# Performance work log

Measured on AMD Instinct MI355X. Metric: run time of the kernel, lower is better.

Reference implementation:

```python
import jax, jax.numpy as jnp
import numpy as np

NEG_INF = -1.0e9  # matches masked_fill_(mask, -1e9)


def setup_inputs() -> dict:
    key = jax.random.key(0)
    k1, k2, k3, k4 = jax.random.split(key, 4)
    B, Tq, Tk, D = 16, 2048, 2048, 1024
    q = jax.random.normal(k1, (B, Tq, D), dtype=jnp.float32)
    k = jax.random.normal(k2, (B, D, Tk), dtype=jnp.float32)  # pre-transposed keys (proj_k output layout)
    v = jax.random.normal(k3, (B, Tk, D), dtype=jnp.float32)
    mask = jax.random.randint(k4, (B, Tq, Tk), 0, 2).astype(jnp.bool_)
    return {"q": q, "k": k, "v": v, "mask": mask}


def reference(q, k, v, mask):
    # scores: [B, Tq, Tk]
    scores = jnp.einsum('bqd,bdk->bqk', q, k)
    scores = jnp.where(mask, jnp.asarray(NEG_INF, scores.dtype), scores)
    att = jax.nn.softmax(scores, axis=-1)
    # dropout is identity in eval mode (training=False)
    context = jnp.einsum('bqk,bkd->bqd', att, v)
    return context
```

## Files before the change

### kernel.cpp

```cpp
#include <hip/hip_runtime.h>
#include <hip/hip_fp16.h>


#define B_    16
#define TQ    2048
#define TK    2048
#define DH    1024
#define BQ    64
#define BT    256
#define DC    128
#define NTHR  512
#define NEG_INF_ -1.0e9f

typedef __attribute__((ext_vector_type(8))) _Float16  f16x8;
typedef __attribute__((ext_vector_type(4))) _Float16  f16x4;
typedef __attribute__((ext_vector_type(4))) float     f32x4;
typedef unsigned int   u32;
typedef unsigned short u16;

__global__ void detect_mask_kernel(const void* __restrict__ mask, int* flag_out) {
    const int tid = threadIdx.x;
    const int*   mi = (const int*)mask;
    const float* mf = (const float*)mask;
    int ok_i = 1, ok_f = 1;
    for (int k = 0; k < 16; ++k) {
        int idx = tid * 16 + k;
        int iv = mi[idx];
        ok_i &= ((iv == 0) | (iv == 1));
        float fv = mf[idx];
        ok_f &= ((fv == 0.0f) | (fv == 1.0f));
    }
    int all_i = __syncthreads_and(ok_i);
    int all_f = __syncthreads_and(ok_f);
    if (tid == 0) flag_out[0] = all_i ? 0 : (all_f ? 1 : 2);
}

template<int CTRL>
__device__ __forceinline__ float dpp_rot(float x) {
    return __int_as_float(__builtin_amdgcn_update_dpp(
        0, __float_as_int(x), CTRL, 0xf, 0xf, false));
}
__device__ __forceinline__ float rowmax16(float v) {
    v = fmaxf(v, dpp_rot<0x128>(v));
    v = fmaxf(v, dpp_rot<0x124>(v));
    v = fmaxf(v, dpp_rot<0x122>(v));
    v = fmaxf(v, dpp_rot<0x121>(v));
    return v;
}
__device__ __forceinline__ float rowsum16(float v) {
    v += dpp_rot<0x128>(v);
    v += dpp_rot<0x124>(v);
    v += dpp_rot<0x122>(v);
    v += dpp_rot<0x121>(v);
    return v;
}

__device__ __forceinline__ void gl_lds16(const u16* g, u16* l) {
    __builtin_amdgcn_global_load_lds(
        (const __attribute__((address_space(1))) u32*)(const void*)g,
        (__attribute__((address_space(3))) u32*)(void*)l, 16, 0, 0);
}

__global__ __launch_bounds__(256)
void prep_q(const float* __restrict__ Q, u16* __restrict__ Qh, u16* __restrict__ Ql) {
    const size_t NU = (size_t)B_ * TQ * (DH / 8);
    for (size_t u = (size_t)blockIdx.x * 256 + threadIdx.x; u < NU;
         u += (size_t)gridDim.x * 256) {
        const int    dk = (int)(u & 127);
        const size_t bq = u >> 7;
        const int    q  = (int)(bq & 2047);
        const int    b  = (int)(bq >> 11);
        const float* src = Q + (bq << 10) + dk * 8;
        float x[8];
        *(float4*)&x[0] = *(const float4*)src;
        *(float4*)&x[4] = *(const float4*)(src + 4);
        f16x8 h, l;
#pragma unroll
        for (int j = 0; j < 8; ++j) {
            h[j] = (_Float16)x[j];
            l[j] = (_Float16)(x[j] - (float)h[j]);
        }
        const int qb = q >> 6, qi = q & 63, c = dk >> 4;
        const int dl = (dk & 15) * 8;
        const size_t tile = ((size_t)(b * 32 + qb) * 8 + c) * 8192;
        const int eoff = (qi * 256 + ((dl * 2) ^ ((qi & 7) << 4))) >> 1;
        *(f16x8*)(Qh + tile + eoff) = h;
        *(f16x8*)(Ql + tile + eoff) = l;
    }
}

__global__ __launch_bounds__(256)
void prep_k(const float* __restrict__ K, u16* __restrict__ Kpk) {
    const size_t NU = (size_t)B_ * (DH / 8) * (TK / 4);
    for (size_t u = (size_t)blockIdx.x * 256 + threadIdx.x; u < NU;
         u += (size_t)gridDim.x * 256) {
        const int    t4  = (int)(u & 511);
        const size_t rem = u >> 9;
        const int    ds  = (int)(rem & 127);
        const int    b   = (int)(rem >> 7);
        const float* src = K + ((size_t)b * DH + ds * 8) * TK + t4 * 4;
        float x[8][4];
#pragma unroll
        for (int j = 0; j < 8; ++j)
            *(float4*)x[j] = *(const float4*)(src + (size_t)j * TK);
        u16* dst = Kpk + (((size_t)b * 128 + ds) * TK + t4 * 4) * 8;
#pragma unroll
        for (int i = 0; i < 4; ++i) {
            f16x8 o;
#pragma unroll
            for (int j = 0; j < 8; ++j) o[j] = (_Float16)x[j][i];
            *(f16x8*)(dst + i * 8) = o;
        }
    }
}

__global__ __launch_bounds__(256)
void prep_v(const float* __restrict__ V, u16* __restrict__ Vpk) {
    const size_t NU = (size_t)B_ * (TK / 8) * (DH / 4);
    for (size_t u = (size_t)blockIdx.x * 256 + threadIdx.x; u < NU;
         u += (size_t)gridDim.x * 256) {
        const int    d4  = (int)(u & 255);
        const size_t rem = u >> 8;
        const int    ts  = (int)(rem & 255);
        const int    b   = (int)(rem >> 8);
        const float* src = V + ((size_t)b * TK + ts * 8) * DH + d4 * 4;
        float x[8][4];
#pragma unroll
        for (int j = 0; j < 8; ++j)
            *(float4*)x[j] = *(const float4*)(src + (size_t)j * DH);
        u16* dst = Vpk + (((size_t)b * 256 + ts) * DH + d4 * 4) * 8;
#pragma unroll
        for (int i = 0; i < 4; ++i) {
            f16x8 o;
#pragma unroll
            for (int j = 0; j < 8; ++j) o[j] = (_Float16)x[j][i];
            *(f16x8*)(dst + i * 8) = o;
        }
    }
}

#define KISSUE(S, SLOT, TCOL) do {                                          \
    const u16* kp_ = Kb + (((size_t)((S) * 4 + g) * TK) + (TCOL)) * 8;      \
    kfrag[SLOT][0] = *(const f16x8*)kp_;                                    \
    kfrag[SLOT][1] = *(const f16x8*)(kp_ + 128);                            \
} while (0)

#define QISSUE(C, CB) do {                                                  \
    const u16* gh_ = Qhb + (size_t)(C) * 8192 + w * 1024 + ln * 8;          \
    const u16* gl_ = Qlb + (size_t)(C) * 8192 + w * 1024 + ln * 8;          \
    gl_lds16(gh_,       &qhs[CB][w * 1024]);                                \
    gl_lds16(gh_ + 512, &qhs[CB][w * 1024 + 512]);                          \
    gl_lds16(gl_,       &qls[CB][w * 1024]);                                \
    gl_lds16(gl_ + 512, &qls[CB][w * 1024 + 512]);                          \
} while (0)

#define QLOAD0(C) do {                                                      \
    const float* qr_ = Qb + (size_t)(tid >> 3) * DH + (C) * DC + (tid & 7) * 16; \
    qreg[0] = *(const float4*)(qr_);      qreg[1] = *(const float4*)(qr_ + 4);   \
    qreg[2] = *(const float4*)(qr_ + 8);  qreg[3] = *(const float4*)(qr_ + 12);  \
} while (0)

#define QSTORE0(CB) do {                                                    \
    const int qq_ = tid >> 3, sw_ = (qq_ & 7) << 4, rowb_ = qq_ * 256;      \
    _Pragma("unroll")                                                       \
    for (int i_ = 0; i_ < 4; ++i_) {                                        \
        const int d_ = (tid & 7) * 16 + i_ * 4;                             \
        const float* qf_ = reinterpret_cast<const float*>(&qreg[i_]);       \
        f16x4 h4_, l4_;                                                     \
        _Pragma("unroll")                                                   \
        for (int e_ = 0; e_ < 4; ++e_) {                                    \
            const _Float16 h_ = (_Float16)qf_[e_];                          \
            h4_[e_] = h_;                                                   \
            l4_[e_] = (_Float16)(qf_[e_] - (float)h_);                      \
        }                                                                   \
        const int off_ = rowb_ + ((d_ * 2) ^ sw_);                          \
        *(f16x4*)((char*)qhs[CB] + off_) = h4_;                             \
        *(f16x4*)((char*)qls[CB] + off_) = l4_;                             \
    }                                                                       \
} while (0)

#define VQUAD(QD, SLOT) do {                                                \
    const size_t ts_ = (size_t)((t0 >> 3) + ((QD) >> 1) * 4 + g);           \
    const u16* vp_ = Vb + (ts_ * DH + w * 128 + ((QD) & 1) * 64 + lx) * 8;  \
    vslot[SLOT][0] = *(const f16x8*)(vp_);                                  \
    vslot[SLOT][1] = *(const f16x8*)(vp_ + 128);                            \
    vslot[SLOT][2] = *(const f16x8*)(vp_ + 256);                            \
    vslot[SLOT][3] = *(const f16x8*)(vp_ + 384);                            \
} while (0)

template<int QMODE>
__global__ __launch_bounds__(NTHR, 2)
void flash_mfma(const float* __restrict__ Q, const u16* __restrict__ Qh,
                const u16* __restrict__ Ql, const u16* __restrict__ Kpk,
                const u16* __restrict__ Vpk, const void* __restrict__ Mask,
                const int* __restrict__ flagp, float* __restrict__ Out) {
    __shared__ u16 qhs[2][BQ * DC];
    __shared__ u16 qls[2][BQ * DC];
    __shared__ u16 pbuf[BQ * BT];
    __shared__ float red [BQ][9];
    __shared__ float red2[BQ][9];
    __shared__ float m_s[BQ], l_s[BQ], alpha_s[BQ];

    const int tid  = threadIdx.x;
    const int w    = tid >> 6;
    const int ln   = tid & 63;
    const int g    = ln >> 4;
    const int lx   = ln & 15;
    const int flag = flagp[0];

    const int lin = blockIdx.y * gridDim.x + blockIdx.x;
    const int nl  = (lin & 7) * 64 + (lin >> 3);
    const int b   = nl >> 5;
    const int q0  = (nl & 31) * BQ;

    const float* Qb  = Q + ((size_t)b * TQ + q0) * DH;
    const u16*   Qhb = Qh + ((size_t)(b * 32 + (q0 >> 6)) * 8) * 8192;
    const u16*   Qlb = Ql + ((size_t)(b * 32 + (q0 >> 6)) * 8) * 8192;
    const u16*   Kb  = Kpk + (size_t)b * DH * TK;
    const u16*   Vb  = Vpk + (size_t)b * TK * DH;

    const f32x4 zero4 = {0.f, 0.f, 0.f, 0.f};
    f32x4 acc[4][8];
#pragma unroll
    for (int mt = 0; mt < 4; ++mt)
#pragma unroll
        for (int nt = 0; nt < 8; ++nt) acc[mt][nt] = zero4;

    f16x8  kfrag[4][2];
    f16x8  vslot[2][4];
    float4 qreg[4];

    if (QMODE == 1) QISSUE(0, 0); else QLOAD0(0);
    KISSUE(0, 0, w * 32 + lx);
    KISSUE(1, 1, w * 32 + lx);

    if (tid < BQ) { m_s[tid] = -3.0e38f; l_s[tid] = 0.0f; }

#pragma unroll 1
    for (int t0 = 0; t0 < TK; t0 += BT) {
        const int tcol = t0 + w * 32 + lx;
        f32x4 sacc[4][2];
#pragma unroll
        for (int mt = 0; mt < 4; ++mt) { sacc[mt][0] = zero4; sacc[mt][1] = zero4; }

#pragma unroll 1
        for (int c = 0; c < 8; ++c) {
            const int cb = c & 1;
            if (QMODE == 0) {
                QSTORE0(cb);
                if (c < 7) QLOAD0(c + 1);
                asm volatile("s_waitcnt lgkmcnt(0)" ::: "memory");
            } else {
                asm volatile("s_waitcnt vmcnt(0)" ::: "memory");
            }
            __builtin_amdgcn_sched_barrier(0);
            __builtin_amdgcn_s_barrier();
            __builtin_amdgcn_sched_barrier(0);
            if (QMODE == 1 && c < 7) QISSUE(c + 1, cb ^ 1);
#pragma unroll
            for (int ks = 0; ks < 4; ++ks) {
                const int s2 = c * 4 + ks + 2;
                if (s2 < 32) KISSUE(s2, (ks + 2) & 3, tcol);
                const int kloc = (ks * 32 + g * 8) * 2;
                __builtin_amdgcn_s_setprio(1);
#pragma unroll
                for (int mt = 0; mt < 4; ++mt) {
                    const int row = mt * 16 + lx;
                    const int off = row * 256 + (kloc ^ ((row & 7) << 4));
                    const f16x8 aqh = *(const f16x8*)((const char*)qhs[cb] + off);
                    const f16x8 aql = *(const f16x8*)((const char*)qls[cb] + off);
                    sacc[mt][0] = __builtin_amdgcn_mfma_f32_16x16x32_f16(aqh, kfrag[ks & 3][0], sacc[mt][0], 0, 0, 0);
                    sacc[mt][0] = __builtin_amdgcn_mfma_f32_16x16x32_f16(aql, kfrag[ks & 3][0], sacc[mt][0], 0, 0, 0);
                    sacc[mt][1] = __builtin_amdgcn_mfma_f32_16x16x32_f16(aqh, kfrag[ks & 3][1], sacc[mt][1], 0, 0, 0);
                    sacc[mt][1] = __builtin_amdgcn_mfma_f32_16x16x32_f16(aql, kfrag[ks & 3][1], sacc[mt][1], 0, 0, 0);
                }
                __builtin_amdgcn_s_setprio(0);
            }
        }

        float rmx[4][4];
#pragma unroll
        for (int mt = 0; mt < 4; ++mt)
#pragma unroll
        for (int r = 0; r < 4; ++r) {
            const int row = mt * 16 + g * 4 + r;
            const size_t mrow = ((size_t)(b * TQ + q0 + row)) * TK + tcol;
            bool mk0, mk1;
            if (flag == 0) {
                const int* Mi = (const int*)Mask;
                mk0 = Mi[mrow] != 0;        mk1 = Mi[mrow + 16] != 0;
            } else if (flag == 1) {
                const float* Mf = (const float*)Mask;
                mk0 = Mf[mrow] != 0.0f;     mk1 = Mf[mrow + 16] != 0.0f;
            } else {
                const unsigned char* Mu = (const unsigned char*)Mask;
                mk0 = Mu[mrow] != 0;        mk1 = Mu[mrow + 16] != 0;
            }
            if (mk0) sacc[mt][0][r] = NEG_INF_;
            if (mk1) sacc[mt][1][r] = NEG_INF_;
            rmx[mt][r] = rowmax16(fmaxf(sacc[mt][0][r], sacc[mt][1][r]));
        }
        if (lx == 0) {
#pragma unroll
            for (int mt = 0; mt < 4; ++mt)
#pragma unroll
            for (int r = 0; r < 4; ++r)
                red[mt * 16 + g * 4 + r][w] = rmx[mt][r];
        }
        __syncthreads();
        if (tid < BQ) {
            float m8 = red[tid][0];
#pragma unroll
            for (int k = 1; k < 8; ++k) m8 = fmaxf(m8, red[tid][k]);
            const float mo = m_s[tid];
            const float mn = fmaxf(mo, m8);
            m_s[tid]     = mn;
            alpha_s[tid] = __expf(mo - mn);
        }
        __syncthreads();
#pragma unroll
        for (int mt = 0; mt < 4; ++mt)
#pragma unroll
        for (int r = 0; r < 4; ++r) {
            const int row = mt * 16 + g * 4 + r;
            const float mn = m_s[row];
            const float p0 = __expf(sacc[mt][0][r] - mn);
            const float p1 = __expf(sacc[mt][1][r] - mn);
            const int rb = row * (BT * 2);
            const int sw = (row & 7) << 4;
            *(_Float16*)((char*)pbuf + rb + (((w * 32 + lx) * 2) ^ sw))      = (_Float16)p0;
            *(_Float16*)((char*)pbuf + rb + (((w * 32 + 16 + lx) * 2) ^ sw)) = (_Float16)p1;
            const float rs = rowsum16(p0 + p1);
            if (lx == 0) red2[row][w] = rs;
        }
        __syncthreads();

        if (t0 + BT < TK) {
            if (QMODE == 1) QISSUE(0, 0); else QLOAD0(0);
            KISSUE(0, 0, tcol + BT);
            KISSUE(1, 1, tcol + BT);
        }
        VQUAD(0, 0);
        VQUAD(1, 1);

        if (tid < BQ) {
            float s8 = red2[tid][0];
#pragma unroll
            for (int k = 1; k < 8; ++k) s8 += red2[tid][k];
            l_s[tid] = l_s[tid] * alpha_s[tid] + s8;
        }
#pragma unroll
        for (int mt = 0; mt < 4; ++mt)
#pragma unroll
        for (int r = 0; r < 4; ++r) {
            const float a = alpha_s[mt * 16 + g * 4 + r];
#pragma unroll
            for (int nt = 0; nt < 8; ++nt) acc[mt][nt][r] *= a;
        }

#pragma unroll 1
        for (int tc = 0; tc < 8; ++tc) {
            f16x8 ap[4];
#pragma unroll
            for (int mt = 0; mt < 4; ++mt) {
                const int row = mt * 16 + lx;
                const int off = row * (BT * 2) + (((tc * 32 + g * 8) * 2) ^ ((row & 7) << 4));
                ap[mt] = *(const f16x8*)((const char*)pbuf + off);
            }
#pragma unroll
            for (int h = 0; h < 2; ++h) {
                __builtin_amdgcn_s_setprio(1);
#pragma unroll
                for (int n = 0; n < 4; ++n) {
                    const int nt = h * 4 + n;
#pragma unroll
                    for (int mt = 0; mt < 4; ++mt)
                        acc[mt][nt] = __builtin_amdgcn_mfma_f32_16x16x32_f16(ap[mt], vslot[h][n], acc[mt][nt], 0, 0, 0);
                }
                __builtin_amdgcn_s_setprio(0);
                const int qd = tc * 2 + h + 2;
                if (qd < 16) {
                    if (h == 0) VQUAD(qd, 0); else VQUAD(qd, 1);
                }
            }
        }
    }

    __syncthreads();
#pragma unroll
    for (int mt = 0; mt < 4; ++mt)
#pragma unroll
    for (int r = 0; r < 4; ++r) {
        const int row = mt * 16 + g * 4 + r;
        const float inv = 1.0f / l_s[row];
        float* orow = Out + ((size_t)(b * TQ + q0 + row)) * DH + w * 128 + lx;
#pragma unroll
        for (int nt = 0; nt < 8; ++nt)
            orow[nt * 16] = acc[mt][nt][r] * inv;
    }
}

#define LOADK_(TCOL, D0, R0, R1) do {                                       \
    const float* kp_ = Kb + (size_t)((D0) + g * 8) * TK + (TCOL);           \
    _Pragma("unroll")                                                       \
    for (int j_ = 0; j_ < 8; ++j_) {                                        \
        (R0)[j_] = kp_[(size_t)j_ * TK];                                    \
        (R1)[j_] = kp_[(size_t)j_ * TK + 16];                               \
    }                                                                       \
} while (0)
#define KCVT_(SRC, DST) do {                                                \
    _Pragma("unroll")                                                       \
    for (int j_ = 0; j_ < 8; ++j_) (DST)[j_] = (_Float16)(SRC)[j_];         \
} while (0)
#define LQLOAD_(DC_) do {                                                   \
    const float* qrow_ = Qb + (size_t)(tid >> 3) * DH + (DC_) + (tid & 7) * 16; \
    qreg[0] = *(const float4*)(qrow_ + 0);  qreg[1] = *(const float4*)(qrow_ + 4); \
    qreg[2] = *(const float4*)(qrow_ + 8);  qreg[3] = *(const float4*)(qrow_ + 12); \
} while (0)
#define LQSTORE_(CB) do {                                                   \
    const int qq_ = tid >> 3, sw_ = (qq_ & 7) << 4, rowb_ = qq_ * (DC * 2); \
    _Pragma("unroll")                                                       \
    for (int i_ = 0; i_ < 4; ++i_) {                                        \
        const int d_ = (tid & 7) * 16 + i_ * 4;                             \
        const float* qf_ = reinterpret_cast<const float*>(&qreg[i_]);       \
        f16x4 h4_, l4_;                                                     \
        _Pragma("unroll")                                                   \
        for (int e_ = 0; e_ < 4; ++e_) {                                    \
            const _Float16 h_ = (_Float16)qf_[e_];                          \
            h4_[e_] = h_;  l4_[e_] = (_Float16)(qf_[e_] - (float)h_);       \
        }                                                                   \
        const int off_ = rowb_ + ((d_ * 2) ^ sw_);                          \
        *(f16x4*)((char*)smu.qk.qh[CB] + off_) = h4_;                       \
        *(f16x4*)((char*)smu.qk.ql[CB] + off_) = l4_;                       \
    }                                                                       \
} while (0)
#define LVLOAD_(T0_, TC_) do {                                              \
    const int tb4_ = (tid & 7) * 4;                                         \
    const float* Vc_ = Vb + (size_t)((T0_) + (TC_) * 32 + tb4_) * DH;       \
    _Pragma("unroll")                                                       \
    for (int it_ = 0; it_ < 4; ++it_) {                                     \
        const int d4_ = (tid >> 3) * 4 + it_ * 256;                         \
        vr[it_][0] = *(const float4*)(Vc_ + 0 * DH + d4_);                  \
        vr[it_][1] = *(const float4*)(Vc_ + 1 * DH + d4_);                  \
        vr[it_][2] = *(const float4*)(Vc_ + 2 * DH + d4_);                  \
        vr[it_][3] = *(const float4*)(Vc_ + 3 * DH + d4_);                  \
    }                                                                       \
} while (0)
#define LVSTORE_() do {                                                     \
    const int tb4_ = (tid & 7) * 4;                                         \
    _Pragma("unroll")                                                       \
    for (int it_ = 0; it_ < 4; ++it_) {                                     \
        const int d4_ = (tid >> 3) * 4 + it_ * 256;                         \
        const float* f0_ = reinterpret_cast<const float*>(&vr[it_][0]);     \
        const float* f1_ = reinterpret_cast<const float*>(&vr[it_][1]);     \
        const float* f2_ = reinterpret_cast<const float*>(&vr[it_][2]);     \
        const float* f3_ = reinterpret_cast<const float*>(&vr[it_][3]);     \
        _Pragma("unroll")                                                   \
        for (int i_ = 0; i_ < 4; ++i_) {                                    \
            f16x4 hv_;                                                      \
            hv_[0] = (_Float16)f0_[i_];  hv_[1] = (_Float16)f1_[i_];        \
            hv_[2] = (_Float16)f2_[i_];  hv_[3] = (_Float16)f3_[i_];        \
            *(f16x4*)((char*)smu.vst + (size_t)(d4_ + i_) * 80 + tb4_ * 2) = hv_; \
        }                                                                   \
    }                                                                       \
} while (0)

__global__ __launch_bounds__(NTHR, 2)
void flash_attn_legacy(const float* __restrict__ Q, const float* __restrict__ K,
                       const float* __restrict__ V, const void* __restrict__ Mask,
                       const int* __restrict__ flagp, float* __restrict__ Out) {
    __shared__ union {
        struct { u16 qh[2][BQ * DC]; u16 ql[2][BQ * DC]; } qk;
        u16 vst[DH * 40];
    } smu;
    __shared__ u16 pbuf[BQ * BT];
    __shared__ float red[BQ][9], red2[BQ][9];
    __shared__ float m_s[BQ], l_s[BQ], alpha_s[BQ];

    const int tid = threadIdx.x, w = tid >> 6, ln = tid & 63;
    const int g = ln >> 4, lx = ln & 15, flag = flagp[0];
    const int lin = blockIdx.y * gridDim.x + blockIdx.x;
    const int nl = (lin & 7) * 64 + (lin >> 3);
    const int b = nl >> 5, q0 = (nl & 31) * BQ;
    const float* Qb = Q + ((size_t)b * TQ + q0) * DH;
    const float* Kb = K + (size_t)b * DH * TK;
    const float* Vb = V + (size_t)b * TK * DH;
    const f32x4 zero4 = {0.f, 0.f, 0.f, 0.f};
    f32x4 acc[4][8];
#pragma unroll
    for (int mt = 0; mt < 4; ++mt)
#pragma unroll
        for (int nt = 0; nt < 8; ++nt) acc[mt][nt] = zero4;
    float4 qreg[4];  float kr0[2][8], kr1[2][8];  float4 vr[4][4];
    LQLOAD_(0);
    LOADK_(w * 32 + lx, 0, kr0[0], kr1[0]);
    LOADK_(w * 32 + lx, 32, kr0[1], kr1[1]);
    if (tid < BQ) { m_s[tid] = -3.0e38f; l_s[tid] = 0.0f; }
    __syncthreads();
#pragma unroll 1
    for (int t0 = 0; t0 < TK; t0 += BT) {
        const int tcol = t0 + w * 32 + lx;
        f32x4 sacc[4][2];
#pragma unroll
        for (int mt = 0; mt < 4; ++mt) { sacc[mt][0] = zero4; sacc[mt][1] = zero4; }
        __syncthreads();
#pragma unroll 1
        for (int c = 0; c < DH / DC; ++c) {
            const int cb = c & 1;
            LQSTORE_(cb);
            if (c < 7) LQLOAD_(c * DC + DC);
            __syncthreads();
#pragma unroll
            for (int ks = 0; ks < 4; ++ks) {
                f16x8 kh0, kh1;
                KCVT_(kr0[ks & 1], kh0);  KCVT_(kr1[ks & 1], kh1);
                { const int nk = ks + 2, nc = c + (nk >> 2);
                  if (nc < 8) LOADK_(tcol, nc * DC + (nk & 3) * 32, kr0[ks & 1], kr1[ks & 1]); }
                const int kloc = (ks * 32 + g * 8) * 2;
#pragma unroll
                for (int mt = 0; mt < 4; ++mt) {
                    const int row = mt * 16 + lx;
                    const int off = row * (DC * 2) + (kloc ^ ((row & 7) << 4));
                    const f16x8 aqh = *(const f16x8*)((const char*)smu.qk.qh[cb] + off);
                    const f16x8 aql = *(const f16x8*)((const char*)smu.qk.ql[cb] + off);
                    sacc[mt][0] = __builtin_amdgcn_mfma_f32_16x16x32_f16(aqh, kh0, sacc[mt][0], 0, 0, 0);
                    sacc[mt][0] = __builtin_amdgcn_mfma_f32_16x16x32_f16(aql, kh0, sacc[mt][0], 0, 0, 0);
                    sacc[mt][1] = __builtin_amdgcn_mfma_f32_16x16x32_f16(aqh, kh1, sacc[mt][1], 0, 0, 0);
                    sacc[mt][1] = __builtin_amdgcn_mfma_f32_16x16x32_f16(aql, kh1, sacc[mt][1], 0, 0, 0);
                }
            }
        }
        LVLOAD_(t0, 0);
        float rmx[4][4];
#pragma unroll
        for (int mt = 0; mt < 4; ++mt)
#pragma unroll
        for (int r = 0; r < 4; ++r) {
            const int row = mt * 16 + g * 4 + r;
            const size_t mrow = ((size_t)(b * TQ + q0 + row)) * TK + tcol;
            bool mk0, mk1;
            if (flag == 0) { const int* Mi = (const int*)Mask; mk0 = Mi[mrow] != 0; mk1 = Mi[mrow + 16] != 0; }
            else if (flag == 1) { const float* Mf = (const float*)Mask; mk0 = Mf[mrow] != 0.0f; mk1 = Mf[mrow + 16] != 0.0f; }
            else { const unsigned char* Mu = (const unsigned char*)Mask; mk0 = Mu[mrow] != 0; mk1 = Mu[mrow + 16] != 0; }
            if (mk0) sacc[mt][0][r] = NEG_INF_;
            if (mk1) sacc[mt][1][r] = NEG_INF_;
            rmx[mt][r] = rowmax16(fmaxf(sacc[mt][0][r], sacc[mt][1][r]));
        }
        if (lx == 0) {
#pragma unroll
            for (int mt = 0; mt < 4; ++mt)
#pragma unroll
            for (int r = 0; r < 4; ++r) red[mt * 16 + g * 4 + r][w] = rmx[mt][r];
        }
        __syncthreads();
        if (tid < BQ) {
            float m8 = red[tid][0];
#pragma unroll
            for (int k = 1; k < 8; ++k) m8 = fmaxf(m8, red[tid][k]);
            const float mo = m_s[tid], mn = fmaxf(mo, m8);
            m_s[tid] = mn;  alpha_s[tid] = __expf(mo - mn);
        }
        __syncthreads();
#pragma unroll
        for (int mt = 0; mt < 4; ++mt)
#pragma unroll
        for (int r = 0; r < 4; ++r) {
            const int row = mt * 16 + g * 4 + r;
            const float mn = m_s[row];
            const float p0 = __expf(sacc[mt][0][r] - mn);
            const float p1 = __expf(sacc[mt][1][r] - mn);
            const int rb = row * (BT * 2), sw = (row & 7) << 4;
            *(_Float16*)((char*)pbuf + rb + (((w * 32 + lx) * 2) ^ sw)) = (_Float16)p0;
            *(_Float16*)((char*)pbuf + rb + (((w * 32 + 16 + lx) * 2) ^ sw)) = (_Float16)p1;
            const float rs = rowsum16(p0 + p1);
            if (lx == 0) red2[row][w] = rs;
        }
        __syncthreads();
        if (tid < BQ) {
            float s8 = red2[tid][0];
#pragma unroll
            for (int k = 1; k < 8; ++k) s8 += red2[tid][k];
            l_s[tid] = l_s[tid] * alpha_s[tid] + s8;
        }
#pragma unroll
        for (int mt = 0; mt < 4; ++mt)
#pragma unroll
        for (int r = 0; r < 4; ++r) {
            const float a = alpha_s[mt * 16 + g * 4 + r];
#pragma unroll
            for (int nt = 0; nt < 8; ++nt) acc[mt][nt][r] *= a;
        }
#pragma unroll 1
        for (int tc = 0; tc < BT / 32; ++tc) {
            __syncthreads();
            LVSTORE_();
            if (tc < 7) { LVLOAD_(t0, tc + 1); }
            else if (t0 + BT < TK) {
                LQLOAD_(0);
                LOADK_(t0 + BT + w * 32 + lx, 0, kr0[0], kr1[0]);
                LOADK_(t0 + BT + w * 32 + lx, 32, kr0[1], kr1[1]);
            }
            __syncthreads();
            f16x8 ap[4];
#pragma unroll
            for (int mt = 0; mt < 4; ++mt) {
                const int row = mt * 16 + lx;
                const int off = row * (BT * 2) + (((tc * 32 + g * 8) * 2) ^ ((row & 7) << 4));
                ap[mt] = *(const f16x8*)((const char*)pbuf + off);
            }
#pragma unroll
            for (int nt = 0; nt < 8; ++nt) {
                const int vrow = w * 128 + nt * 16 + lx;
                const f16x8 bv = *(const f16x8*)((const char*)smu.vst + (size_t)vrow * 80 + g * 16);
#pragma unroll
                for (int mt = 0; mt < 4; ++mt)
                    acc[mt][nt] = __builtin_amdgcn_mfma_f32_16x16x32_f16(ap[mt], bv, acc[mt][nt], 0, 0, 0);
            }
        }
    }
    __syncthreads();
#pragma unroll
    for (int mt = 0; mt < 4; ++mt)
#pragma unroll
    for (int r = 0; r < 4; ++r) {
        const int row = mt * 16 + g * 4 + r;
        const float inv = 1.0f / l_s[row];
        float* orow = Out + ((size_t)(b * TQ + q0 + row)) * DH + w * 128 + lx;
#pragma unroll
        for (int nt = 0; nt < 8; ++nt) orow[nt * 16] = acc[mt][nt][r] * inv;
    }
}

extern "C" void kernel_launch(void* const* d_in, const int* in_sizes, int n_in,
                              void* d_out, int out_size, void* d_ws, size_t ws_size,
                              hipStream_t stream) {
    const float* q    = (const float*)d_in[0];
    const float* k    = (const float*)d_in[1];
    const float* v    = (const float*)d_in[2];
    const void*  mask = d_in[3];
    float* out = (float*)d_out;
    int* flag = (int*)d_ws;

    hipLaunchKernelGGL(detect_mask_kernel, dim3(1), dim3(256), 0, stream, mask, flag);

    const size_t SZH = (size_t)B_ * TQ * DH * sizeof(u16);
    char* wsb = (char*)d_ws + 1024;
    dim3 grid(TQ / BQ, B_);

    if (ws_size >= 4 * SZH + 1024) {
        u16* Kpk = (u16*)wsb;
        u16* Vpk = (u16*)(wsb + SZH);
        u16* Qh  = (u16*)(wsb + 2 * SZH);
        u16* Ql  = (u16*)(wsb + 3 * SZH);
        hipLaunchKernelGGL(prep_k, dim3(2048), dim3(256), 0, stream, k, Kpk);
        hipLaunchKernelGGL(prep_v, dim3(2048), dim3(256), 0, stream, v, Vpk);
        hipLaunchKernelGGL(prep_q, dim3(2048), dim3(256), 0, stream, q, Qh, Ql);
        hipLaunchKernelGGL(flash_mfma<1>, grid, dim3(NTHR), 0, stream,
                           q, Qh, Ql, Kpk, Vpk, mask, flag, out);
    } else if (ws_size >= 2 * SZH + 1024) {
        u16* Kpk = (u16*)wsb;
        u16* Vpk = (u16*)(wsb + SZH);
        hipLaunchKernelGGL(prep_k, dim3(2048), dim3(256), 0, stream, k, Kpk);
        hipLaunchKernelGGL(prep_v, dim3(2048), dim3(256), 0, stream, v, Vpk);
        hipLaunchKernelGGL(flash_mfma<0>, grid, dim3(NTHR), 0, stream,
                           q, (const u16*)nullptr, (const u16*)nullptr,
                           Kpk, Vpk, mask, flag, out);
    } else {
        hipLaunchKernelGGL(flash_attn_legacy, grid, dim3(NTHR), 0, stream,
                           q, k, v, mask, flag, out);
    }
}
```

Baseline: 1.495 ms.

## Fuse prep kernels into one launch, bit-pack mask, relax waits and barriers

Merges the K, V and Q prep kernels into a single block-partitioned prep_all launch and adds a fourth partition that packs the boolean mask into 32-bit bitmasks. The attention kernel then reads one packed word per row and tile instead of a byte per score element. V loads are issued earlier, before the softmax, so they overlap with it. Full vmcnt(0) waits become partial waits, and __syncthreads is replaced by an LDS-only wait plus barrier. This cuts launch overhead and mask traffic, at the cost of extra workspace, an extra pass over the mask, and more register pressure from the early V loads and mask words.

```diff
diff --git a/kernel.cpp b/kernel.cpp
--- a/kernel.cpp
+++ b/kernel.cpp
@@ -61,80 +61,132 @@
         (__attribute__((address_space(3))) u32*)(void*)l, 16, 0, 0);
 }
 
+#define PBK 434
+#define PBV 434
+#define PBQ 580
+#define PBM 600
+#define PBLK (PBK + PBV + PBQ + PBM)
+
 __global__ __launch_bounds__(256)
-void prep_q(const float* __restrict__ Q, u16* __restrict__ Qh, u16* __restrict__ Ql) {
-    const size_t NU = (size_t)B_ * TQ * (DH / 8);
-    for (size_t u = (size_t)blockIdx.x * 256 + threadIdx.x; u < NU;
-         u += (size_t)gridDim.x * 256) {
-        const int    dk = (int)(u & 127);
-        const size_t bq = u >> 7;
-        const int    q  = (int)(bq & 2047);
-        const int    b  = (int)(bq >> 11);
-        const float* src = Q + (bq << 10) + dk * 8;
-        float x[8];
-        *(float4*)&x[0] = *(const float4*)src;
-        *(float4*)&x[4] = *(const float4*)(src + 4);
-        f16x8 h, l;
-#pragma unroll
-        for (int j = 0; j < 8; ++j) {
-            h[j] = (_Float16)x[j];
-            l[j] = (_Float16)(x[j] - (float)h[j]);
-        }
-        const int qb = q >> 6, qi = q & 63, c = dk >> 4;
-        const int dl = (dk & 15) * 8;
-        const size_t tile = ((size_t)(b * 32 + qb) * 8 + c) * 8192;
-        const int eoff = (qi * 256 + ((dl * 2) ^ ((qi & 7) << 4))) >> 1;
-        *(f16x8*)(Qh + tile + eoff) = h;
-        *(f16x8*)(Ql + tile + eoff) = l;
-    }
-}
-
-__global__ __launch_bounds__(256)
-void prep_k(const float* __restrict__ K, u16* __restrict__ Kpk) {
-    const size_t NU = (size_t)B_ * (DH / 8) * (TK / 4);
-    for (size_t u = (size_t)blockIdx.x * 256 + threadIdx.x; u < NU;
-         u += (size_t)gridDim.x * 256) {
-        const int    t4  = (int)(u & 511);
-        const size_t rem = u >> 9;
-        const int    ds  = (int)(rem & 127);
-        const int    b   = (int)(rem >> 7);
-        const float* src = K + ((size_t)b * DH + ds * 8) * TK + t4 * 4;
-        float x[8][4];
-#pragma unroll
-        for (int j = 0; j < 8; ++j)
-            *(float4*)x[j] = *(const float4*)(src + (size_t)j * TK);
-        u16* dst = Kpk + (((size_t)b * 128 + ds) * TK + t4 * 4) * 8;
-#pragma unroll
-        for (int i = 0; i < 4; ++i) {
-            f16x8 o;
-#pragma unroll
-            for (int j = 0; j < 8; ++j) o[j] = (_Float16)x[j][i];
-            *(f16x8*)(dst + i * 8) = o;
-        }
-    }
-}
-
-__global__ __launch_bounds__(256)
-void prep_v(const float* __restrict__ V, u16* __restrict__ Vpk) {
-    const size_t NU = (size_t)B_ * (TK / 8) * (DH / 4);
-    for (size_t u = (size_t)blockIdx.x * 256 + threadIdx.x; u < NU;
-         u += (size_t)gridDim.x * 256) {
-        const int    d4  = (int)(u & 255);
-        const size_t rem = u >> 8;
-        const int    ts  = (int)(rem & 255);
-        const int    b   = (int)(rem >> 8);
-        const float* src = V + ((size_t)b * TK + ts * 8) * DH + d4 * 4;
-        float x[8][4];
-#pragma unroll
-        for (int j = 0; j < 8; ++j)
-            *(float4*)x[j] = *(const float4*)(src + (size_t)j * DH);
-        u16* dst = Vpk + (((size_t)b * 256 + ts) * DH + d4 * 4) * 8;
-#pragma unroll
-        for (int i = 0; i < 4; ++i) {
-            f16x8 o;
-#pragma unroll
-            for (int j = 0; j < 8; ++j) o[j] = (_Float16)x[j][i];
-            *(f16x8*)(dst + i * 8) = o;
+void prep_all(const float* __restrict__ Q, const float* __restrict__ K,
+              const float* __restrict__ V, const void* __restrict__ Mask,
+              const int* __restrict__ flagp,
+              u16* __restrict__ Kpk, u16* __restrict__ Vpk,
+              u16* __restrict__ Qh,  u16* __restrict__ Ql,
+              u32* __restrict__ Mpk) {
+    const int blk = blockIdx.x, tid = threadIdx.x;
+    if (blk < PBK) {
+        const size_t NU = (size_t)B_ * (DH / 8) * (TK / 4);
+        for (size_t u = (size_t)blk * 256 + tid; u < NU; u += (size_t)PBK * 256) {
+            const int    t4  = (int)(u & 511);
+            const size_t rem = u >> 9;
+            const int    ds  = (int)(rem & 127);
+            const int    b   = (int)(rem >> 7);
+            const float* src = K + ((size_t)b * DH + ds * 8) * TK + t4 * 4;
+            float x[8][4];
+#pragma unroll
+            for (int j = 0; j < 8; ++j)
+                *(float4*)x[j] = *(const float4*)(src + (size_t)j * TK);
+            u16* dst = Kpk + (((size_t)b * 128 + ds) * TK + t4 * 4) * 8;
+#pragma unroll
+            for (int i = 0; i < 4; ++i) {
+                f16x8 o;
+#pragma unroll
+                for (int j = 0; j < 8; ++j) o[j] = (_Float16)x[j][i];
+                *(f16x8*)(dst + i * 8) = o;
+            }
+        }
+    } else if (blk < PBK + PBV) {
+        const int rb = blk - PBK;
+        const size_t NU = (size_t)B_ * (TK / 8) * (DH / 4);
+        for (size_t u = (size_t)rb * 256 + tid; u < NU; u += (size_t)PBV * 256) {
+            const int    d4  = (int)(u & 255);
+            const size_t rem = u >> 8;
+            const int    ts  = (int)(rem & 255);
+            const int    b   = (int)(rem >> 8);
+            const float* src = V + ((size_t)b * TK + ts * 8) * DH + d4 * 4;
+            float x[8][4];
+#pragma unroll
+            for (int j = 0; j < 8; ++j)
+                *(float4*)x[j] = *(const float4*)(src + (size_t)j * DH);
+            u16* dst = Vpk + (((size_t)b * 256 + ts) * DH + d4 * 4) * 8;
+#pragma unroll
+            for (int i = 0; i < 4; ++i) {
+                f16x8 o;
+#pragma unroll
+                for (int j = 0; j < 8; ++j) o[j] = (_Float16)x[j][i];
+                *(f16x8*)(dst + i * 8) = o;
+            }
+        }
+    } else if (blk < PBK + PBV + PBQ) {
+        if (Qh == nullptr) return;
+        const int rb = blk - PBK - PBV;
+        const size_t NU = (size_t)B_ * TQ * (DH / 8);
+        for (size_t u = (size_t)rb * 256 + tid; u < NU; u += (size_t)PBQ * 256) {
+            const int    dk = (int)(u & 127);
+            const size_t bq = u >> 7;
+            const int    q  = (int)(bq & 2047);
+            const int    b  = (int)(bq >> 11);
+            const float* src = Q + (bq << 10) + dk * 8;
+            float x[8];
+            *(float4*)&x[0] = *(const float4*)src;
+            *(float4*)&x[4] = *(const float4*)(src + 4);
+            f16x8 h, l;
+#pragma unroll
+            for (int j = 0; j < 8; ++j) {
+                h[j] = (_Float16)x[j];
+                l[j] = (_Float16)(x[j] - (float)h[j]);
+            }
+            const int qb = q >> 6, qi = q & 63, c = dk >> 4;
+            const int dl = (dk & 15) * 8;
+            const size_t tile = ((size_t)(b * 32 + qb) * 8 + c) * 8192;
+            const int eoff = (qi * 256 + ((dl * 2) ^ ((qi & 7) << 4))) >> 1;
+            *(f16x8*)(Qh + tile + eoff) = h;
+            *(f16x8*)(Ql + tile + eoff) = l;
+        }
+    } else {
+        if (Mpk == nullptr) return;
+        const int rb = blk - PBK - PBV - PBQ;
+        const int flag = flagp[0];
+        const size_t NU = (size_t)B_ * TQ * (TK / 32);
+        for (size_t u = (size_t)rb * 256 + tid; u < NU; u += (size_t)PBM * 256) {
+            u32 bits = 0;
+            if (flag == 0) {
+                const int4* p = (const int4*)Mask + u * 8;
+#pragma unroll
+                for (int j = 0; j < 8; ++j) {
+                    int4 x = p[j];
+                    bits |= (x.x != 0 ? 1u : 0u) << (4 * j + 0);
+                    bits |= (x.y != 0 ? 1u : 0u) << (4 * j + 1);
+                    bits |= (x.z != 0 ? 1u : 0u) << (4 * j + 2);
+                    bits |= (x.w != 0 ? 1u : 0u) << (4 * j + 3);
+                }
+            } else if (flag == 1) {
+                const float4* p = (const float4*)Mask + u * 8;
+#pragma unroll
+                for (int j = 0; j < 8; ++j) {
+                    float4 x = p[j];
+                    bits |= (x.x != 0.f ? 1u : 0u) << (4 * j + 0);
+                    bits |= (x.y != 0.f ? 1u : 0u) << (4 * j + 1);
+                    bits |= (x.z != 0.f ? 1u : 0u) << (4 * j + 2);
+                    bits |= (x.w != 0.f ? 1u : 0u) << (4 * j + 3);
+                }
+            } else {
+                const uint4* p = (const uint4*)Mask + u * 2;
+#pragma unroll
+                for (int j = 0; j < 2; ++j) {
+                    uint4 x = p[j];
+                    u32 w0 = x.x, w1 = x.y, w2 = x.z, w3 = x.w;
+#pragma unroll
+                    for (int k = 0; k < 4; ++k) {
+                        bits |= (((w0 >> (8 * k)) & 0xffu) ? 1u : 0u) << (j * 16 + 0 + k);
+                        bits |= (((w1 >> (8 * k)) & 0xffu) ? 1u : 0u) << (j * 16 + 4 + k);
+                        bits |= (((w2 >> (8 * k)) & 0xffu) ? 1u : 0u) << (j * 16 + 8 + k);
+                        bits |= (((w3 >> (8 * k)) & 0xffu) ? 1u : 0u) << (j * 16 + 12 + k);
+                    }
+                }
+            }
+            Mpk[u] = bits;
         }
     }
 }
@@ -188,12 +240,20 @@
     vslot[SLOT][3] = *(const f16x8*)(vp_ + 384);                            \
 } while (0)
 
-template<int QMODE>
+#define LBAR() do {                                                         \
+    asm volatile("s_waitcnt lgkmcnt(0)" ::: "memory");                      \
+    __builtin_amdgcn_sched_barrier(0);                                      \
+    __builtin_amdgcn_s_barrier();                                           \
+    __builtin_amdgcn_sched_barrier(0);                                      \
+} while (0)
+
+template<int QMODE, int MMODE>
 __global__ __launch_bounds__(NTHR, 2)
 void flash_mfma(const float* __restrict__ Q, const u16* __restrict__ Qh,
                 const u16* __restrict__ Ql, const u16* __restrict__ Kpk,
                 const u16* __restrict__ Vpk, const void* __restrict__ Mask,
-                const int* __restrict__ flagp, float* __restrict__ Out) {
+                const u32* __restrict__ Mpk, const int* __restrict__ flagp,
+                float* __restrict__ Out) {
     __shared__ u16 qhs[2][BQ * DC];
     __shared__ u16 qls[2][BQ * DC];
     __shared__ u16 pbuf[BQ * BT];
@@ -251,7 +311,8 @@
                 if (c < 7) QLOAD0(c + 1);
                 asm volatile("s_waitcnt lgkmcnt(0)" ::: "memory");
             } else {
-                asm volatile("s_waitcnt vmcnt(0)" ::: "memory");
+                if (c == 0) asm volatile("s_waitcnt vmcnt(4)" ::: "memory");
+                else        asm volatile("s_waitcnt vmcnt(8)" ::: "memory");
             }
             __builtin_amdgcn_sched_barrier(0);
             __builtin_amdgcn_s_barrier();
@@ -278,23 +339,40 @@
             }
         }
 
+        VQUAD(0, 0);
+        VQUAD(1, 1);
+
+        u32 mb[4][4];
+        if (MMODE == 1) {
+            const u32* Mp = Mpk + (size_t)(b * TQ + q0) * 64 + (t0 >> 5) + w;
+#pragma unroll
+            for (int mt = 0; mt < 4; ++mt)
+#pragma unroll
+            for (int r = 0; r < 4; ++r)
+                mb[mt][r] = Mp[(size_t)(mt * 16 + g * 4 + r) * 64];
+        }
         float rmx[4][4];
 #pragma unroll
         for (int mt = 0; mt < 4; ++mt)
 #pragma unroll
         for (int r = 0; r < 4; ++r) {
-            const int row = mt * 16 + g * 4 + r;
-            const size_t mrow = ((size_t)(b * TQ + q0 + row)) * TK + tcol;
             bool mk0, mk1;
-            if (flag == 0) {
-                const int* Mi = (const int*)Mask;
-                mk0 = Mi[mrow] != 0;        mk1 = Mi[mrow + 16] != 0;
-            } else if (flag == 1) {
-                const float* Mf = (const float*)Mask;
-                mk0 = Mf[mrow] != 0.0f;     mk1 = Mf[mrow + 16] != 0.0f;
+            if (MMODE == 1) {
+                mk0 = (mb[mt][r] >> lx) & 1u;
+                mk1 = (mb[mt][r] >> (16 + lx)) & 1u;
             } else {
-                const unsigned char* Mu = (const unsigned char*)Mask;
-                mk0 = Mu[mrow] != 0;        mk1 = Mu[mrow + 16] != 0;
+                const int row = mt * 16 + g * 4 + r;
+                const size_t mrow = ((size_t)(b * TQ + q0 + row)) * TK + tcol;
+                if (flag == 0) {
+                    const int* Mi = (const int*)Mask;
+                    mk0 = Mi[mrow] != 0;        mk1 = Mi[mrow + 16] != 0;
+                } else if (flag == 1) {
+                    const float* Mf = (const float*)Mask;
+                    mk0 = Mf[mrow] != 0.0f;     mk1 = Mf[mrow + 16] != 0.0f;
+                } else {
+                    const unsigned char* Mu = (const unsigned char*)Mask;
+                    mk0 = Mu[mrow] != 0;        mk1 = Mu[mrow + 16] != 0;
+                }
             }
             if (mk0) sacc[mt][0][r] = NEG_INF_;
             if (mk1) sacc[mt][1][r] = NEG_INF_;
@@ -307,7 +385,7 @@
             for (int r = 0; r < 4; ++r)
                 red[mt * 16 + g * 4 + r][w] = rmx[mt][r];
         }
-        __syncthreads();
+        LBAR();
         if (tid < BQ) {
             float m8 = red[tid][0];
 #pragma unroll
@@ -317,7 +395,7 @@
             m_s[tid]     = mn;
             alpha_s[tid] = __expf(mo - mn);
         }
-        __syncthreads();
+        LBAR();
 #pragma unroll
         for (int mt = 0; mt < 4; ++mt)
 #pragma unroll
@@ -333,15 +411,13 @@
             const float rs = rowsum16(p0 + p1);
             if (lx == 0) red2[row][w] = rs;
         }
-        __syncthreads();
+        LBAR();
 
         if (t0 + BT < TK) {
             if (QMODE == 1) QISSUE(0, 0); else QLOAD0(0);
             KISSUE(0, 0, tcol + BT);
             KISSUE(1, 1, tcol + BT);
         }
-        VQUAD(0, 0);
-        VQUAD(1, 1);
 
         if (tid < BQ) {
             float s8 = red2[tid][0];
@@ -643,28 +719,39 @@
 
     hipLaunchKernelGGL(detect_mask_kernel, dim3(1), dim3(256), 0, stream, mask, flag);
 
-    const size_t SZH = (size_t)B_ * TQ * DH * sizeof(u16);
+    const size_t SZH  = (size_t)B_ * TQ * DH * sizeof(u16);
+    const size_t MPKB = (size_t)B_ * TQ * (TK / 32) * sizeof(u32);
     char* wsb = (char*)d_ws + 1024;
     dim3 grid(TQ / BQ, B_);
 
-    if (ws_size >= 4 * SZH + 1024) {
+    if (ws_size >= 4 * SZH + MPKB + 1024) {
         u16* Kpk = (u16*)wsb;
         u16* Vpk = (u16*)(wsb + SZH);
         u16* Qh  = (u16*)(wsb + 2 * SZH);
         u16* Ql  = (u16*)(wsb + 3 * SZH);
-        hipLaunchKernelGGL(prep_k, dim3(2048), dim3(256), 0, stream, k, Kpk);
-        hipLaunchKernelGGL(prep_v, dim3(2048), dim3(256), 0, stream, v, Vpk);
-        hipLaunchKernelGGL(prep_q, dim3(2048), dim3(256), 0, stream, q, Qh, Ql);
-        hipLaunchKernelGGL(flash_mfma<1>, grid, dim3(NTHR), 0, stream,
-                           q, Qh, Ql, Kpk, Vpk, mask, flag, out);
+        u32* Mpk = (u32*)(wsb + 4 * SZH);
+        hipLaunchKernelGGL(prep_all, dim3(PBLK), dim3(256), 0, stream,
+                           q, k, v, mask, flag, Kpk, Vpk, Qh, Ql, Mpk);
+        hipLaunchKernelGGL((flash_mfma<1, 1>), grid, dim3(NTHR), 0, stream,
+                           q, Qh, Ql, Kpk, Vpk, mask, Mpk, flag, out);
+    } else if (ws_size >= 4 * SZH + 1024) {
+        u16* Kpk = (u16*)wsb;
+        u16* Vpk = (u16*)(wsb + SZH);
+        u16* Qh  = (u16*)(wsb + 2 * SZH);
+        u16* Ql  = (u16*)(wsb + 3 * SZH);
+        hipLaunchKernelGGL(prep_all, dim3(PBLK), dim3(256), 0, stream,
+                           q, k, v, mask, flag, Kpk, Vpk, Qh, Ql, (u32*)nullptr);
+        hipLaunchKernelGGL((flash_mfma<1, 0>), grid, dim3(NTHR), 0, stream,
+                           q, Qh, Ql, Kpk, Vpk, mask, (const u32*)nullptr, flag, out);
     } else if (ws_size >= 2 * SZH + 1024) {
         u16* Kpk = (u16*)wsb;
         u16* Vpk = (u16*)(wsb + SZH);
-        hipLaunchKernelGGL(prep_k, dim3(2048), dim3(256), 0, stream, k, Kpk);
-        hipLaunchKernelGGL(prep_v, dim3(2048), dim3(256), 0, stream, v, Vpk);
-        hipLaunchKernelGGL(flash_mfma<0>, grid, dim3(NTHR), 0, stream,
+        hipLaunchKernelGGL(prep_all, dim3(PBLK), dim3(256), 0, stream,
+                           q, k, v, mask, flag, Kpk, Vpk, (u16*)nullptr, (u16*)nullptr,
+                           (u32*)nullptr);
+        hipLaunchKernelGGL((flash_mfma<0, 0>), grid, dim3(NTHR), 0, stream,
                            q, (const u16*)nullptr, (const u16*)nullptr,
-                           Kpk, Vpk, mask, flag, out);
+                           Kpk, Vpk, mask, (const u32*)nullptr, flag, out);
     } else {
         hipLaunchKernelGGL(flash_attn_legacy, grid, dim3(NTHR), 0, stream,
                            q, k, v, mask, flag, out);
```

New measurement: 1.529 ms. 1.02x slower.
